# Optimization experiments

Hardware: AMD Instinct MI355X
Metric: run time of the kernel (lower is better)

## Reference

```python
import jax, jax.numpy as jnp
import numpy as np

B, S, H, A = 64, 200, 256, 16
CAPS_LAYERS = 3
NEG = -1e9
LN_EPS = 1e-12


def _layernorm(x, g, b):
    mu = jnp.mean(x, axis=-1, keepdims=True)
    var = jnp.mean(jnp.square(x - mu), axis=-1, keepdims=True)
    return (x - mu) / jnp.sqrt(var + LN_EPS) * g + b


def setup_inputs() -> dict:
    key = jax.random.key(0)
    ks = jax.random.split(key, 10)
    s = 0.02  # initializer_range
    return {
        "item_emb": jax.random.normal(ks[0], (B, S, H), jnp.float32),
        "item_seq": jax.random.randint(ks[1], (B, S), 0, 50000),
        "time_seq": jax.random.randint(ks[2], (B, S, 2), 0, 14),
        "W_lin": s * jax.random.normal(ks[3], (H, H), jnp.float32),
        "b_lin": jnp.zeros((H,), jnp.float32),
        "aspect_embs": s * jax.random.normal(ks[4], (A, H), jnp.float32),
        "pos_emb": s * jax.random.normal(ks[5], (S, H), jnp.float32),
        "tdt_emb": s * jax.random.normal(ks[6], (14, H), jnp.float32),
        "tdn_emb": s * jax.random.normal(ks[7], (14, H), jnp.float32),
        "Wa1": s * jax.random.normal(ks[8], (H, H), jnp.float32),
        "ba1": jnp.zeros((H,), jnp.float32),
        "Wa2": s * jax.random.normal(ks[9], (H,), jnp.float32),
        "ba2": jnp.zeros((1,), jnp.float32),
        "ln_g": jnp.ones((H,), jnp.float32),
        "ln_b": jnp.zeros((H,), jnp.float32),
    }


def reference(item_emb, item_seq, time_seq, W_lin, b_lin, aspect_embs,
              pos_emb, tdt_emb, tdn_emb, Wa1, ba1, Wa2, ba2, ln_g, ln_b):
    b, s = item_emb.shape[0], item_emb.shape[1]
    pad = item_seq == 0  # [B,S]

    # ---- TimeAwareAttention (seq_output has a singleton neighbor dim in torch) ----
    td = tdt_emb[time_seq[:, :, 0]] + tdn_emb[time_seq[:, :, 1]]       # [B,S,H]
    tma_in = pos_emb[None, :s] + item_emb + td                          # [B,S,H]
    h = tma_in @ Wa1 + ba1
    h = jnp.where(h >= 0, h, 0.01 * h)                                  # LeakyReLU
    w = h @ Wa2 + ba2[0]                                                # [B,S]
    w = jnp.where(pad, NEG, w)
    tma = jax.nn.softmax(w, axis=-1)                                    # [B,S]

    # ---- gating (eval: clean gates) ----
    gates = jnp.einsum('bsh,ah->bsa', item_emb, aspect_embs)            # [B,S,A]
    idx = jnp.argmax(gates, axis=-1)                                    # topk k=1, [B,S]

    src = jnp.where(pad, 0.0, 1.0)
    counts = jnp.zeros((b, A), jnp.float32).at[jnp.arange(b)[:, None], idx].add(src)
    aspect_mask = counts == 0                                           # [B,A]

    # ---- item transform (dropout = identity in eval) ----
    moe = _layernorm(jnp.tanh(item_emb @ W_lin + b_lin) + item_emb, ln_g, ln_b)  # [B,S,H]

    # ---- capsule routing ----
    bij = gates
    cap = jnp.broadcast_to(aspect_embs[None], (b, A, H))
    for _ in range(CAPS_LAYERS):
        cij = jnp.where(aspect_mask[:, None, :], NEG, bij)
        cij = jax.nn.softmax(cij, axis=-1)
        cij = jnp.where(pad[:, :, None], 0.0, cij)                      # [B,S,A]
        cap = jnp.einsum('bsa,bsh,bs->bah', cij, moe, tma)              # [B,A,H]
        n2 = jnp.sum(jnp.square(cap), axis=-1, keepdims=True)
        cap = n2 / (1.0 + n2) / jnp.sqrt(n2 + 1e-9) * cap               # squash
        bij = bij + jnp.einsum('bsh,bah->bsa', moe, cap)

    # ---- gather activated interests / activation positions ----
    activated = cap[jnp.arange(b)[:, None], idx]                        # [B,S,H]
    seq_pos = jnp.where(pad, 0, jnp.arange(1, s + 1)[None, :]).astype(jnp.float32)
    act_mat = jnp.full((b, s, A), -1.0, jnp.float32)
    act_mat = act_mat.at[jnp.arange(b)[:, None], jnp.arange(s)[None, :], idx].set(seq_pos)
    act_mat = jnp.where(pad[:, :, None], -1.0, act_mat)
    max_pos = jnp.max(act_mat, axis=1)                                  # [B,A]
    aspects_item_idx = jnp.where(max_pos > -1.0, max_pos - 1.0, max_pos)

    gates_sm = jax.nn.softmax(gates, axis=-1)
    return (cap, gates_sm, aspect_mask, activated, aspects_item_idx, idx[:, :, None])
```

## Files before the change

kernel.cpp:

```cpp
#include <hip/hip_runtime.h>

#define B_ 64
#define S_ 200
#define H_ 256
#define A_ 16
#define M_ (B_*S_)
#define NEGV (-1000000000.0f)

typedef unsigned short ushortT;
typedef __attribute__((ext_vector_type(8))) short short8;
typedef __attribute__((ext_vector_type(4))) float f32x4;

__device__ __forceinline__ ushortT bf16u(float f) {
  unsigned int u = __builtin_bit_cast(unsigned int, f);
  unsigned int r = (u + 0x7fffu + ((u >> 16) & 1u)) >> 16;
  return (ushortT)r;
}
__device__ __forceinline__ float bf2f(ushortT u) {
  unsigned int v = ((unsigned int)u) << 16;
  return __builtin_bit_cast(float, v);
}

__global__ __launch_bounds__(256) void prepT_kernel(
    const float* __restrict__ Wa1, const float* __restrict__ W_lin,
    ushortT* __restrict__ Wa1T, ushortT* __restrict__ WlinT)
{
  __shared__ float T[64*65];
  const int blk = blockIdx.x, t = threadIdx.x;
  int wsel = blk >> 4;
  int tile = blk & 15;
  const float* W = wsel ? W_lin : Wa1;
  ushortT* WT = wsel ? WlinT : Wa1T;
  int tr = (tile >> 2) * 64, tc = (tile & 3) * 64;
  #pragma unroll
  for (int p = 0; p < 16; ++p) {
    int r = p*4 + (t >> 6);
    int c = t & 63;
    T[c*65 + r] = W[(tr + r)*H_ + tc + c];
  }
  __syncthreads();
  #pragma unroll
  for (int p = 0; p < 16; ++p) {
    int n = p*4 + (t >> 6);
    int k = t & 63;
    WT[(tc + n)*H_ + tr + k] = bf16u(T[n*65 + k]);
  }
}

#define ASTR 264
__global__ __launch_bounds__(512) void gemmx_kernel(
    const float* __restrict__ item, const int* __restrict__ iseq,
    const int* __restrict__ tseq, const float* __restrict__ pos,
    const float* __restrict__ tdt, const float* __restrict__ tdn,
    const float* __restrict__ asp,
    const ushortT* __restrict__ Wa1T, const ushortT* __restrict__ WlinT,
    const float* __restrict__ ba1, const float* __restrict__ Wa2,
    const float* __restrict__ ba2, const float* __restrict__ b_lin,
    const float* __restrict__ g_ln, const float* __restrict__ b_ln,
    float* __restrict__ w_out, ushortT* __restrict__ moe_outB,
    float* __restrict__ graw, float* __restrict__ gates_sm,
    float* __restrict__ idxf)
{
  __shared__ __align__(16) ushortT smem[74752];
  __shared__ int sL[64], ttL[64], tnL[64];
  __shared__ float wp[2][64], ln1[2][64], ln2[2][64], mus[64], rss[64];

  const int t = threadIdx.x;

  if (blockIdx.x >= 200) {
    float* aspl = (float*)smem;
    float* gLs  = aspl + 16*260;
    const int m0 = (blockIdx.x - 200) * 32;
    #pragma unroll
    for (int i = 0; i < 2; ++i) {
      int e = t + 512*i;
      int r = e >> 6, c = e & 63;
      *(float4*)&aspl[r*260 + 4*c] = *(const float4*)&asp[r*H_ + 4*c];
    }
    __syncthreads();
    const int r = t >> 4, a = t & 15;
    const int m = m0 + r;
    float g = 0.f;
    #pragma unroll 8
    for (int k4 = 0; k4 < 64; ++k4) {
      float4 xv = *(const float4*)&item[(size_t)m*H_ + 4*k4];
      float4 av = *(const float4*)&aspl[a*260 + 4*k4];
      g += xv.x*av.x + xv.y*av.y + xv.z*av.z + xv.w*av.w;
    }
    gLs[r*20 + a] = g;
    __syncthreads();
    if (t < 128) {
      int rr = t >> 2, q = t & 3;
      float4 gv;
      gv.x = gLs[rr*20 + 4*q + 0]; gv.y = gLs[rr*20 + 4*q + 1];
      gv.z = gLs[rr*20 + 4*q + 2]; gv.w = gLs[rr*20 + 4*q + 3];
      *(float4*)&graw[(m0+rr)*A_ + 4*q] = gv;
    }
    {
      float v = g;
      float mx = v;
      #pragma unroll
      for (int mk = 1; mk < 16; mk <<= 1) mx = fmaxf(mx, __shfl_xor(mx, mk));
      float e = expf(v - mx);
      float sm = e;
      #pragma unroll
      for (int mk = 1; mk < 16; mk <<= 1) sm += __shfl_xor(sm, mk);
      gates_sm[(size_t)m*A_ + a] = e / sm;
    }
    if (t < 32) {
      float best = gLs[t*20]; int bi = 0;
      #pragma unroll
      for (int aa = 1; aa < 16; ++aa) {
        float v = gLs[t*20 + aa];
        if (v > best) { best = v; bi = aa; }
      }
      idxf[m0 + t] = (float)bi;
    }
    return;
  }

  ushortT* Atma = smem;
  ushortT* Aitm = smem + 16896;
  ushortT* Bbuf = smem + 33792;

  const int m0 = blockIdx.x * 64;
  const int lane = t & 63, w = t >> 6;
  const int g = w >> 2, wl = w & 3;
  const int wm = wl >> 1, wn = wl & 1;
  const int col = lane & 15;
  const int rg  = lane >> 4;

  if (t < 64) {
    int m = m0 + t;
    sL[t]  = m % S_;
    ttL[t] = tseq[2*m];
    tnL[t] = tseq[2*m+1];
  }
  __syncthreads();

  const int arow = t >> 3;
  const int ac4  = (t & 7) * 4;
  const int nr   = t >> 1;
  const int kh   = (t & 1) * 16;
  const int srow = sL[arow], trow = ttL[arow], nrow = tnL[arow];

  float4 pi = *(const float4*)&item[(size_t)(m0+arow)*H_ + ac4];
  float4 pp = *(const float4*)&pos[srow*H_ + ac4];
  float4 pt = *(const float4*)&tdt[trow*H_ + ac4];
  float4 pn = *(const float4*)&tdn[nrow*H_ + ac4];
  uint4 b0a = *(const uint4*)&Wa1T[(size_t)nr*H_ + kh];
  uint4 b0b = *(const uint4*)&Wa1T[(size_t)nr*H_ + kh + 8];
  uint4 b1a = *(const uint4*)&WlinT[(size_t)nr*H_ + kh];
  uint4 b1b = *(const uint4*)&WlinT[(size_t)nr*H_ + kh + 8];

  f32x4 acc[2][8];
  #pragma unroll
  for (int r = 0; r < 2; ++r)
    #pragma unroll
    for (int q = 0; q < 8; ++q) acc[r][q] = (f32x4){0.f,0.f,0.f,0.f};

  {
    union { ushortT u[4]; uint2 v; } ci, ct;
    ci.u[0] = bf16u(pi.x); ci.u[1] = bf16u(pi.y);
    ci.u[2] = bf16u(pi.z); ci.u[3] = bf16u(pi.w);
    ct.u[0] = bf16u(pi.x + pp.x + pt.x + pn.x);
    ct.u[1] = bf16u(pi.y + pp.y + pt.y + pn.y);
    ct.u[2] = bf16u(pi.z + pp.z + pt.z + pn.z);
    ct.u[3] = bf16u(pi.w + pp.w + pt.w + pn.w);
    *(uint2*)&Aitm[arow*ASTR + ac4] = ci.v;
    *(uint2*)&Atma[arow*ASTR + ac4] = ct.v;
    *(uint4*)&Bbuf[0*10240 + nr*40 + kh]     = b0a;
    *(uint4*)&Bbuf[0*10240 + nr*40 + kh + 8] = b0b;
    *(uint4*)&Bbuf[2*10240 + nr*40 + kh]     = b1a;
    *(uint4*)&Bbuf[2*10240 + nr*40 + kh + 8] = b1b;
  }
  __syncthreads();

  #pragma unroll
  for (int ks = 0; ks < 8; ++ks) {
    const int k0 = ks*32;
    if (ks < 7) {
      const int k1 = k0 + 32;
      pi = *(const float4*)&item[(size_t)(m0+arow)*H_ + k1 + ac4];
      pp = *(const float4*)&pos[srow*H_ + k1 + ac4];
      pt = *(const float4*)&tdt[trow*H_ + k1 + ac4];
      pn = *(const float4*)&tdn[nrow*H_ + k1 + ac4];
      b0a = *(const uint4*)&Wa1T[(size_t)nr*H_ + k1 + kh];
      b0b = *(const uint4*)&Wa1T[(size_t)nr*H_ + k1 + kh + 8];
      b1a = *(const uint4*)&WlinT[(size_t)nr*H_ + k1 + kh];
      b1b = *(const uint4*)&WlinT[(size_t)nr*H_ + k1 + kh + 8];
    }
    {
      const ushortT* Ab = g ? Aitm : Atma;
      const ushortT* Bb = Bbuf + (g*2 + (ks & 1))*10240;
      short8 af0 = *(const short8*)&Ab[(wm*32 + col)*ASTR + k0 + rg*8];
      short8 af1 = *(const short8*)&Ab[(wm*32 + 16 + col)*ASTR + k0 + rg*8];
      #pragma unroll
      for (int q = 0; q < 8; ++q) {
        short8 bf = *(const short8*)&Bb[(wn*128 + q*16 + col)*40 + rg*8];
        acc[0][q] = __builtin_amdgcn_mfma_f32_16x16x32_bf16(af0, bf, acc[0][q], 0, 0, 0);
        acc[1][q] = __builtin_amdgcn_mfma_f32_16x16x32_bf16(af1, bf, acc[1][q], 0, 0, 0);
      }
    }
    if (ks < 7) {
      const int k1 = k0 + 32;
      const int p = (ks + 1) & 1;
      union { ushortT u[4]; uint2 v; } ci, ct;
      ci.u[0] = bf16u(pi.x); ci.u[1] = bf16u(pi.y);
      ci.u[2] = bf16u(pi.z); ci.u[3] = bf16u(pi.w);
      ct.u[0] = bf16u(pi.x + pp.x + pt.x + pn.x);
      ct.u[1] = bf16u(pi.y + pp.y + pt.y + pn.y);
      ct.u[2] = bf16u(pi.z + pp.z + pt.z + pn.z);
      ct.u[3] = bf16u(pi.w + pp.w + pt.w + pn.w);
      *(uint2*)&Aitm[arow*ASTR + k1 + ac4] = ci.v;
      *(uint2*)&Atma[arow*ASTR + k1 + ac4] = ct.v;
      *(uint4*)&Bbuf[(0*2+p)*10240 + nr*40 + kh]     = b0a;
      *(uint4*)&Bbuf[(0*2+p)*10240 + nr*40 + kh + 8] = b0b;
      *(uint4*)&Bbuf[(1*2+p)*10240 + nr*40 + kh]     = b1a;
      *(uint4*)&Bbuf[(1*2+p)*10240 + nr*40 + kh + 8] = b1b;
    }
    __syncthreads();
  }

  float glv[8], bbv[8];
  if (g == 0) {
    float bav[8], wav[8];
    #pragma unroll
    for (int q = 0; q < 8; ++q) {
      int n = wn*128 + q*16 + col;
      bav[q] = ba1[n]; wav[q] = Wa2[n];
    }
    #pragma unroll
    for (int r = 0; r < 2; ++r)
      #pragma unroll
      for (int j = 0; j < 4; ++j) {
        float p = 0.f;
        #pragma unroll
        for (int q = 0; q < 8; ++q) {
          float h = acc[r][q][j] + bav[q];
          h = (h >= 0.f) ? h : 0.01f*h;
          p += h * wav[q];
        }
        #pragma unroll
        for (int mk = 1; mk < 16; mk <<= 1) p += __shfl_xor(p, mk);
        if (col == 0) wp[wn][wm*32 + r*16 + rg*4 + j] = p;
      }
  } else {
    float blv[8];
    #pragma unroll
    for (int q = 0; q < 8; ++q) {
      int n = wn*128 + q*16 + col;
      blv[q] = b_lin[n]; glv[q] = g_ln[n]; bbv[q] = b_ln[n];
    }
    #pragma unroll
    for (int r = 0; r < 2; ++r)
      #pragma unroll
      for (int j = 0; j < 4; ++j) {
        int row = wm*32 + r*16 + rg*4 + j;
        float s1 = 0.f, s2 = 0.f;
        #pragma unroll
        for (int q = 0; q < 8; ++q) {
          int n = wn*128 + q*16 + col;
          float vv = tanhf(acc[r][q][j] + blv[q]) + bf2f(Aitm[row*ASTR + n]);
          acc[r][q][j] = vv; s1 += vv; s2 += vv*vv;
        }
        #pragma unroll
        for (int mk = 1; mk < 16; mk <<= 1) {
          s1 += __shfl_xor(s1, mk);
          s2 += __shfl_xor(s2, mk);
        }
        if (col == 0) { ln1[wn][row] = s1; ln2[wn][row] = s2; }
      }
  }
  __syncthreads();
  if (t < 64) {
    int row = t, m = m0 + row;
    w_out[m] = (iseq[m] == 0) ? NEGV : (wp[0][row] + wp[1][row] + ba2[0]);
  } else if (t < 128) {
    int row = t - 64;
    float s1 = ln1[0][row] + ln1[1][row];
    float s2 = ln2[0][row] + ln2[1][row];
    float mu  = s1 * (1.0f/H_);
    float var = s2 * (1.0f/H_) - mu*mu;
    mus[row] = mu;
    rss[row] = 1.0f / sqrtf(fmaxf(var, 0.f) + 1e-12f);
  }
  __syncthreads();
  if (g == 1) {
    #pragma unroll
    for (int r = 0; r < 2; ++r)
      #pragma unroll
      for (int j = 0; j < 4; ++j) {
        int row = wm*32 + r*16 + rg*4 + j;
        int m = m0 + row;
        float mu = mus[row], rs = rss[row];
        #pragma unroll
        for (int q = 0; q < 8; ++q) {
          int n = wn*128 + q*16 + col;
          moe_outB[(size_t)m*H_ + n] = bf16u((acc[r][q][j] - mu)*rs*glv[q] + bbv[q]);
        }
      }
  }
}

__device__ __forceinline__ float blk_max(float v, float* red) {
  #pragma unroll
  for (int mk = 32; mk; mk >>= 1) v = fmaxf(v, __shfl_xor(v, mk));
  int t = threadIdx.x;
  if ((t & 63) == 0) red[t >> 6] = v;
  __syncthreads();
  if (t < 64) {
    float x = (t < 16) ? red[t] : -3.0e38f;
    #pragma unroll
    for (int mk = 8; mk; mk >>= 1) x = fmaxf(x, __shfl_xor(x, mk));
    if (t == 0) red[0] = x;
  }
  __syncthreads();
  float r = red[0];
  __syncthreads();
  return r;
}

__device__ __forceinline__ float blk_sum(float v, float* red) {
  #pragma unroll
  for (int mk = 32; mk; mk >>= 1) v += __shfl_xor(v, mk);
  int t = threadIdx.x;
  if ((t & 63) == 0) red[t >> 6] = v;
  __syncthreads();
  if (t < 64) {
    float x = (t < 16) ? red[t] : 0.f;
    #pragma unroll
    for (int mk = 8; mk; mk >>= 1) x += __shfl_xor(x, mk);
    if (t == 0) red[0] = x;
  }
  __syncthreads();
  float r = red[0];
  __syncthreads();
  return r;
}

#define WGSTR 232
#define CBSTR 260
#define CLSTR 252

__global__ __launch_bounds__(1024) void phaseC_kernel(
    const int* __restrict__ iseq, const float* __restrict__ w_in,
    const ushortT* __restrict__ moeB, const float* __restrict__ idxf,
    const float* __restrict__ graw,
    float* __restrict__ cap_out,
    float* __restrict__ mask_out,
    float* __restrict__ aidx_out)
{
  __shared__ ushortT moeTr[57344];
  __shared__ ushortT wgtT[16*WGSTR];
  __shared__ ushortT capB[16*CBSTR];
  __shared__ float bij[4032];
  __shared__ float n2p[16*17];
  __shared__ float n2s[16];
  __shared__ float tmaL[S_];
  __shared__ float red[16];
  __shared__ float maskf[A_];
  __shared__ int counts[A_], maxpos[A_];
  __shared__ int idxl[S_];
  __shared__ int padl[S_];

  const int t = threadIdx.x;
  const int b = blockIdx.x;
  const int base = b * S_;
  const int lane = t & 63, w = t >> 6;
  const int la = lane & 15, lg = lane >> 4;

  #pragma unroll
  for (int u = 0; u < 4; ++u) {
    int e = t + 1024*u;
    if (e < 3584) {
      int ht = e & 15, s = e >> 4;
      int ks = s >> 5, s4l = (s >> 2) & 7, sr = s & 3;
      int bp = (s4l & 1) ? 4 + (s4l >> 1) : (s4l >> 1);
      int li = ((ht*7 + ks)*8 + bp)*64 + sr*16;
      if (s < S_) {
        const ushortT* gp = &moeB[((size_t)(base + s))*H_ + ht*16];
        *(uint4*)&moeTr[li]     = *(const uint4*)gp;
        *(uint4*)&moeTr[li + 8] = *(const uint4*)(gp + 8);
      } else {
        uint4 z = {0,0,0,0};
        *(uint4*)&moeTr[li] = z; *(uint4*)&moeTr[li + 8] = z;
      }
    }
  }
  if (t < 512) {
    int a = t >> 5, s = 200 + (t & 31);
    wgtT[a*WGSTR + s] = 0;
  }

  if (t < A_) { counts[t] = 0; maxpos[t] = -1; }
  float wv = -3.0e38f;
  if (t < S_) {
    int s = t;
    padl[s] = (iseq[base+s] == 0) ? 1 : 0;
    idxl[s] = (int)idxf[base+s];
    wv = w_in[base+s];
    #pragma unroll
    for (int q = 0; q < 4; ++q)
      *(float4*)&bij[s*20 + 4*q] = *(const float4*)&graw[(base+s)*A_ + 4*q];
  }
  __syncthreads();

  short8 a2[7];
  {
    unsigned vA = (unsigned)(w*7168 + lane*8);
    #pragma unroll
    for (int ks = 0; ks < 7; ++ks) {
      long long r0, r1;
      asm volatile(
        "ds_read_b64_tr_b16 %0, %2\n\t"
        "ds_read_b64_tr_b16 %1, %2 offset:512\n\t"
        "s_waitcnt lgkmcnt(0)"
        : "=&v"(r0), "=&v"(r1) : "v"(vA + (unsigned)(ks*1024)) : "memory");
      __builtin_amdgcn_sched_barrier(0);
      union { short8 v; long long q[2]; } uu;
      uu.q[0] = r0; uu.q[1] = r1;
      a2[ks] = uu.v;
    }
  }

  if (t < S_ && !padl[t]) {
    atomicAdd(&counts[idxl[t]], 1);
    atomicMax(&maxpos[idxl[t]], t + 1);
  }
  float mxw = blk_max(wv, red);
  float ev = (t < S_) ? expf(wv - mxw) : 0.f;
  float sw = blk_sum(ev, red);
  if (t < S_) tmaL[t] = ev / sw;
  __syncthreads();
  if (t < A_) {
    int c = counts[t];
    float mkv = (c == 0) ? 1.f : 0.f;
    maskf[t] = mkv;
    mask_out[b*A_ + t] = mkv;
    int mp = maxpos[t];
    aidx_out[b*A_ + t] = (mp > 0) ? (float)(mp - 1) : -1.f;
  }
  __syncthreads();

  for (int iter = 0; iter < 3; ++iter) {
    #pragma unroll
    for (int pass = 0; pass < 4; ++pass) {
      int s = pass*64 + (t >> 4);
      int a = t & 15;
      if (s < S_) {
        float v = bij[s*20 + a];
        v = (maskf[a] > 0.5f) ? NEGV : v;
        float mx = v;
        #pragma unroll
        for (int mk = 1; mk < 16; mk <<= 1) mx = fmaxf(mx, __shfl_xor(mx, mk));
        float e = expf(v - mx);
        float sm = e;
        #pragma unroll
        for (int mk = 1; mk < 16; mk <<= 1) sm += __shfl_xor(sm, mk);
        float sc = (padl[s] ? 0.f : tmaL[s]) / sm;
        wgtT[a*WGSTR + s] = bf16u(e*sc);
      }
    }
    __syncthreads();

    f32x4 acc = (f32x4){0.f,0.f,0.f,0.f};
    #pragma unroll
    for (int ks = 0; ks < 7; ++ks) {
      short8 bf = *(const short8*)&wgtT[la*WGSTR + ks*32 + lg*8];
      acc = __builtin_amdgcn_mfma_f32_16x16x32_bf16(a2[ks], bf, acc, 0, 0, 0);
    }
    {
      float n2 = acc[0]*acc[0] + acc[1]*acc[1] + acc[2]*acc[2] + acc[3]*acc[3];
      n2 += __shfl_xor(n2, 16);
      n2 += __shfl_xor(n2, 32);
      if (lane < 16) n2p[w*17 + lane] = n2;
    }
    __syncthreads();
    if (t < 16) {
      float sv = 0.f;
      #pragma unroll
      for (int w2 = 0; w2 < 16; ++w2) sv += n2p[w2*17 + t];
      n2s[t] = sv / (1.f + sv) / sqrtf(sv + 1e-9f);
    }
    __syncthreads();
    {
      float sc = n2s[la];
      if (iter < 2) {
        #pragma unroll
        for (int r = 0; r < 4; ++r)
          capB[la*CBSTR + w*16 + lg*4 + r] = bf16u(acc[r]*sc);
      } else {
        float* capl = bij;
        #pragma unroll
        for (int r = 0; r < 4; ++r)
          capl[la*CLSTR + w*16 + lg*4 + r] = acc[r]*sc;
      }
    }
    __syncthreads();

    if (iter < 2) {
      if (w < 13) {
        int sR = w*16 + la;
        int ksS = sR >> 5, s4l = (sR >> 2) & 7, sr = sR & 3;
        int bp = (s4l & 1) ? 4 + (s4l >> 1) : (s4l >> 1);
        int laneA = ksS*512 + bp*64 + sr*16 + (lg & 1)*8 + (lg >> 1)*3584;
        f32x4 accS = (f32x4){0.f,0.f,0.f,0.f};
        #pragma unroll
        for (int k4 = 0; k4 < 8; ++k4) {
          short8 am = *(const short8*)&moeTr[laneA + k4*7168];
          short8 bc = *(const short8*)&capB[la*CBSTR + k4*32 + lg*8];
          accS = __builtin_amdgcn_mfma_f32_16x16x32_bf16(am, bc, accS, 0, 0, 0);
        }
        int sW = w*16 + lg*4;
        #pragma unroll
        for (int r = 0; r < 4; ++r)
          if (sW + r < S_) bij[(sW + r)*20 + la] += accS[r];
      }
      __syncthreads();
    }
  }

  {
    const float* capl = bij;
    int a = t >> 6, h4 = t & 63;
    float4 v = *(const float4*)&capl[a*CLSTR + 4*h4];
    *(float4*)&cap_out[((size_t)b*A_ + a)*H_ + 4*h4] = v;
  }
}

__global__ __launch_bounds__(256) void gather_kernel(
    const float* __restrict__ capv, const float* __restrict__ idxf,
    float* __restrict__ act)
{
  int e4 = blockIdx.x * 256 + threadIdx.x;
  int m = e4 >> 6, h4 = e4 & 63;
  int b = m / S_;
  int id = (int)idxf[m];
  float4 v = *(const float4*)&capv[((b*A_) + id)*H_ + 4*h4];
  *(float4*)&act[(size_t)4*e4] = v;
}

extern "C" void kernel_launch(void* const* d_in, const int* in_sizes, int n_in,
                              void* d_out, int out_size, void* d_ws, size_t ws_size,
                              hipStream_t stream) {
  (void)in_sizes; (void)n_in; (void)out_size; (void)ws_size;
  const float* item  = (const float*)d_in[0];
  const int*   iseq  = (const int*)d_in[1];
  const int*   tseq  = (const int*)d_in[2];
  const float* W_lin = (const float*)d_in[3];
  const float* b_lin = (const float*)d_in[4];
  const float* asp   = (const float*)d_in[5];
  const float* pos   = (const float*)d_in[6];
  const float* tdt   = (const float*)d_in[7];
  const float* tdn   = (const float*)d_in[8];
  const float* Wa1   = (const float*)d_in[9];
  const float* ba1   = (const float*)d_in[10];
  const float* Wa2   = (const float*)d_in[11];
  const float* ba2   = (const float*)d_in[12];
  const float* g_ln  = (const float*)d_in[13];
  const float* b_ln  = (const float*)d_in[14];

  float* out    = (float*)d_out;
  float* cap_o  = out;
  float* gate_o = out + 262144;
  float* mask_o = out + 466944;
  float* act_o  = out + 467968;
  float* aidx_o = out + 3744768;
  float* idx_o  = out + 3745792;

  ushortT* moeB  = (ushortT*)d_ws;
  ushortT* Wa1T  = (ushortT*)((char*)d_ws + 6553600);
  ushortT* WlinT = (ushortT*)((char*)d_ws + 6553600 + 131072);
  float*   w_ws  = (float*)((char*)d_ws + 6553600 + 262144);
  float*   graw  = (float*)((char*)d_ws + 6553600 + 262144 + 51200);

  prepT_kernel<<<32, 256, 0, stream>>>(Wa1, W_lin, Wa1T, WlinT);
  gemmx_kernel<<<600, 512, 0, stream>>>(item, iseq, tseq, pos, tdt, tdn, asp,
      Wa1T, WlinT, ba1, Wa2, ba2, b_lin, g_ln, b_ln, w_ws, moeB,
      graw, gate_o, idx_o);
  phaseC_kernel<<<B_, 1024, 0, stream>>>(iseq, w_ws, moeB, idx_o, graw,
      cap_o, mask_o, aidx_o);
  gather_kernel<<<(M_*H_/4)/256, 256, 0, stream>>>(cap_o, idx_o, act_o);
}
```

Before: 60.33 us.

## Fuse gating into GEMM blocks, shrink LDS, fold gather into phaseC

The gating/argmax/softmax work is moved from 400 separate blocks into the tail of each of the 200 GEMM blocks. The A tiles become double-buffered 32-wide K slices instead of full 256-wide rows, which cuts shared memory use. The residual in the epilogue now reads fp32 item from global memory instead of the bf16 LDS copy, which also changes precision slightly. The separate gather kernel is removed and the activated-interest gather is done from LDS at the end of phaseC, saving a launch and a global re-read of cap. The cost is that the gating work now runs serially after the GEMM inside each block, and fewer blocks are launched overall.

Result: faster. 57.95 us (median of 2 runs) (-3.9%).

```diff
diff --git a/kernel.cpp b/kernel.cpp
--- a/kernel.cpp
+++ b/kernel.cpp
@@ -47,8 +47,7 @@
   }
 }
 
-#define ASTR 264
-__global__ __launch_bounds__(512) void gemmx_kernel(
+__global__ __launch_bounds__(512) void fused_kernel(
     const float* __restrict__ item, const int* __restrict__ iseq,
     const int* __restrict__ tseq, const float* __restrict__ pos,
     const float* __restrict__ tdt, const float* __restrict__ tdn,
@@ -61,68 +60,11 @@
     float* __restrict__ graw, float* __restrict__ gates_sm,
     float* __restrict__ idxf)
 {
-  __shared__ __align__(16) ushortT smem[74752];
+  __shared__ __align__(16) ushortT smem[51200];
   __shared__ int sL[64], ttL[64], tnL[64];
   __shared__ float wp[2][64], ln1[2][64], ln2[2][64], mus[64], rss[64];
 
   const int t = threadIdx.x;
-
-  if (blockIdx.x >= 200) {
-    float* aspl = (float*)smem;
-    float* gLs  = aspl + 16*260;
-    const int m0 = (blockIdx.x - 200) * 32;
-    #pragma unroll
-    for (int i = 0; i < 2; ++i) {
-      int e = t + 512*i;
-      int r = e >> 6, c = e & 63;
-      *(float4*)&aspl[r*260 + 4*c] = *(const float4*)&asp[r*H_ + 4*c];
-    }
-    __syncthreads();
-    const int r = t >> 4, a = t & 15;
-    const int m = m0 + r;
-    float g = 0.f;
-    #pragma unroll 8
-    for (int k4 = 0; k4 < 64; ++k4) {
-      float4 xv = *(const float4*)&item[(size_t)m*H_ + 4*k4];
-      float4 av = *(const float4*)&aspl[a*260 + 4*k4];
-      g += xv.x*av.x + xv.y*av.y + xv.z*av.z + xv.w*av.w;
-    }
-    gLs[r*20 + a] = g;
-    __syncthreads();
-    if (t < 128) {
-      int rr = t >> 2, q = t & 3;
-      float4 gv;
-      gv.x = gLs[rr*20 + 4*q + 0]; gv.y = gLs[rr*20 + 4*q + 1];
-      gv.z = gLs[rr*20 + 4*q + 2]; gv.w = gLs[rr*20 + 4*q + 3];
-      *(float4*)&graw[(m0+rr)*A_ + 4*q] = gv;
-    }
-    {
-      float v = g;
-      float mx = v;
-      #pragma unroll
-      for (int mk = 1; mk < 16; mk <<= 1) mx = fmaxf(mx, __shfl_xor(mx, mk));
-      float e = expf(v - mx);
-      float sm = e;
-      #pragma unroll
-      for (int mk = 1; mk < 16; mk <<= 1) sm += __shfl_xor(sm, mk);
-      gates_sm[(size_t)m*A_ + a] = e / sm;
-    }
-    if (t < 32) {
-      float best = gLs[t*20]; int bi = 0;
-      #pragma unroll
-      for (int aa = 1; aa < 16; ++aa) {
-        float v = gLs[t*20 + aa];
-        if (v > best) { best = v; bi = aa; }
-      }
-      idxf[m0 + t] = (float)bi;
-    }
-    return;
-  }
-
-  ushortT* Atma = smem;
-  ushortT* Aitm = smem + 16896;
-  ushortT* Bbuf = smem + 33792;
-
   const int m0 = blockIdx.x * 64;
   const int lane = t & 63, w = t >> 6;
   const int g = w >> 2, wl = w & 3;
@@ -143,6 +85,11 @@
   const int nr   = t >> 1;
   const int kh   = (t & 1) * 16;
   const int srow = sL[arow], trow = ttL[arow], nrow = tnL[arow];
+
+  ushortT* const Atma0 = smem;
+  ushortT* const Aitm0 = smem + 5120;
+  ushortT* const B0b   = smem + 10240;
+  ushortT* const B1b   = smem + 30720;
 
   float4 pi = *(const float4*)&item[(size_t)(m0+arow)*H_ + ac4];
   float4 pp = *(const float4*)&pos[srow*H_ + ac4];
@@ -152,13 +99,6 @@
   uint4 b0b = *(const uint4*)&Wa1T[(size_t)nr*H_ + kh + 8];
   uint4 b1a = *(const uint4*)&WlinT[(size_t)nr*H_ + kh];
   uint4 b1b = *(const uint4*)&WlinT[(size_t)nr*H_ + kh + 8];
-
-  f32x4 acc[2][8];
-  #pragma unroll
-  for (int r = 0; r < 2; ++r)
-    #pragma unroll
-    for (int q = 0; q < 8; ++q) acc[r][q] = (f32x4){0.f,0.f,0.f,0.f};
-
   {
     union { ushortT u[4]; uint2 v; } ci, ct;
     ci.u[0] = bf16u(pi.x); ci.u[1] = bf16u(pi.y);
@@ -167,20 +107,25 @@
     ct.u[1] = bf16u(pi.y + pp.y + pt.y + pn.y);
     ct.u[2] = bf16u(pi.z + pp.z + pt.z + pn.z);
     ct.u[3] = bf16u(pi.w + pp.w + pt.w + pn.w);
-    *(uint2*)&Aitm[arow*ASTR + ac4] = ci.v;
-    *(uint2*)&Atma[arow*ASTR + ac4] = ct.v;
-    *(uint4*)&Bbuf[0*10240 + nr*40 + kh]     = b0a;
-    *(uint4*)&Bbuf[0*10240 + nr*40 + kh + 8] = b0b;
-    *(uint4*)&Bbuf[2*10240 + nr*40 + kh]     = b1a;
-    *(uint4*)&Bbuf[2*10240 + nr*40 + kh + 8] = b1b;
-  }
-  __syncthreads();
+    *(uint2*)&Aitm0[arow*40 + ac4] = ci.v;
+    *(uint2*)&Atma0[arow*40 + ac4] = ct.v;
+    *(uint4*)&B0b[nr*40 + kh]     = b0a;
+    *(uint4*)&B0b[nr*40 + kh + 8] = b0b;
+    *(uint4*)&B1b[nr*40 + kh]     = b1a;
+    *(uint4*)&B1b[nr*40 + kh + 8] = b1b;
+  }
+  __syncthreads();
+
+  f32x4 acc[2][8];
+  #pragma unroll
+  for (int r = 0; r < 2; ++r)
+    #pragma unroll
+    for (int q = 0; q < 8; ++q) acc[r][q] = (f32x4){0.f,0.f,0.f,0.f};
 
   #pragma unroll
   for (int ks = 0; ks < 8; ++ks) {
-    const int k0 = ks*32;
     if (ks < 7) {
-      const int k1 = k0 + 32;
+      const int k1 = (ks + 1) * 32;
       pi = *(const float4*)&item[(size_t)(m0+arow)*H_ + k1 + ac4];
       pp = *(const float4*)&pos[srow*H_ + k1 + ac4];
       pt = *(const float4*)&tdt[trow*H_ + k1 + ac4];
@@ -191,10 +136,11 @@
       b1b = *(const uint4*)&WlinT[(size_t)nr*H_ + k1 + kh + 8];
     }
     {
-      const ushortT* Ab = g ? Aitm : Atma;
-      const ushortT* Bb = Bbuf + (g*2 + (ks & 1))*10240;
-      short8 af0 = *(const short8*)&Ab[(wm*32 + col)*ASTR + k0 + rg*8];
-      short8 af1 = *(const short8*)&Ab[(wm*32 + 16 + col)*ASTR + k0 + rg*8];
+      const int p = ks & 1;
+      const ushortT* Ab = (g ? Aitm0 : Atma0) + p*2560;
+      const ushortT* Bb = (g ? B1b : B0b) + p*10240;
+      short8 af0 = *(const short8*)&Ab[(wm*32 + col)*40 + rg*8];
+      short8 af1 = *(const short8*)&Ab[(wm*32 + 16 + col)*40 + rg*8];
       #pragma unroll
       for (int q = 0; q < 8; ++q) {
         short8 bf = *(const short8*)&Bb[(wn*128 + q*16 + col)*40 + rg*8];
@@ -203,7 +149,6 @@
       }
     }
     if (ks < 7) {
-      const int k1 = k0 + 32;
       const int p = (ks + 1) & 1;
       union { ushortT u[4]; uint2 v; } ci, ct;
       ci.u[0] = bf16u(pi.x); ci.u[1] = bf16u(pi.y);
@@ -212,14 +157,25 @@
       ct.u[1] = bf16u(pi.y + pp.y + pt.y + pn.y);
       ct.u[2] = bf16u(pi.z + pp.z + pt.z + pn.z);
       ct.u[3] = bf16u(pi.w + pp.w + pt.w + pn.w);
-      *(uint2*)&Aitm[arow*ASTR + k1 + ac4] = ci.v;
-      *(uint2*)&Atma[arow*ASTR + k1 + ac4] = ct.v;
-      *(uint4*)&Bbuf[(0*2+p)*10240 + nr*40 + kh]     = b0a;
-      *(uint4*)&Bbuf[(0*2+p)*10240 + nr*40 + kh + 8] = b0b;
-      *(uint4*)&Bbuf[(1*2+p)*10240 + nr*40 + kh]     = b1a;
-      *(uint4*)&Bbuf[(1*2+p)*10240 + nr*40 + kh + 8] = b1b;
+      *(uint2*)&(Aitm0 + p*2560)[arow*40 + ac4] = ci.v;
+      *(uint2*)&(Atma0 + p*2560)[arow*40 + ac4] = ct.v;
+      ushortT* B0w = B0b + p*10240;
+      ushortT* B1w = B1b + p*10240;
+      *(uint4*)&B0w[nr*40 + kh]     = b0a;
+      *(uint4*)&B0w[nr*40 + kh + 8] = b0b;
+      *(uint4*)&B1w[nr*40 + kh]     = b1a;
+      *(uint4*)&B1w[nr*40 + kh + 8] = b1b;
     }
     __syncthreads();
+  }
+
+  float* aspl = (float*)smem;
+  float* gL   = (float*)smem + 4160;
+  #pragma unroll
+  for (int i = 0; i < 2; ++i) {
+    int e = t + 512*i;
+    int r = e >> 6, c = e & 63;
+    *(float4*)&aspl[r*260 + 4*c] = *(const float4*)&asp[r*H_ + 4*c];
   }
 
   float glv[8], bbv[8];
@@ -261,7 +217,7 @@
         #pragma unroll
         for (int q = 0; q < 8; ++q) {
           int n = wn*128 + q*16 + col;
-          float vv = tanhf(acc[r][q][j] + blv[q]) + bf2f(Aitm[row*ASTR + n]);
+          float vv = tanhf(acc[r][q][j] + blv[q]) + item[(size_t)(m0+row)*H_ + n];
           acc[r][q][j] = vv; s1 += vv; s2 += vv*vv;
         }
         #pragma unroll
@@ -301,6 +257,47 @@
         }
       }
   }
+
+  {
+    const int r8 = t >> 3, a2 = (t & 7) * 2;
+    const int m = m0 + r8;
+    float ga = 0.f, gb = 0.f;
+    #pragma unroll 8
+    for (int k4 = 0; k4 < 64; ++k4) {
+      float4 xv = *(const float4*)&item[(size_t)m*H_ + 4*k4];
+      float4 a0 = *(const float4*)&aspl[a2*260 + 4*k4];
+      float4 a1 = *(const float4*)&aspl[(a2+1)*260 + 4*k4];
+      ga += xv.x*a0.x + xv.y*a0.y + xv.z*a0.z + xv.w*a0.w;
+      gb += xv.x*a1.x + xv.y*a1.y + xv.z*a1.z + xv.w*a1.w;
+    }
+    gL[r8*20 + a2]     = ga;
+    gL[r8*20 + a2 + 1] = gb;
+  }
+  __syncthreads();
+  if (t < 64) {
+    float row[16];
+    #pragma unroll
+    for (int a = 0; a < 16; ++a) row[a] = gL[t*20 + a];
+    float best = row[0]; int bi = 0;
+    #pragma unroll
+    for (int a = 1; a < 16; ++a)
+      if (row[a] > best) { best = row[a]; bi = a; }
+    idxf[m0 + t] = (float)bi;
+    float mx = row[0];
+    #pragma unroll
+    for (int a = 1; a < 16; ++a) mx = fmaxf(mx, row[a]);
+    float ex[16], sm = 0.f;
+    #pragma unroll
+    for (int a = 0; a < 16; ++a) { ex[a] = expf(row[a] - mx); sm += ex[a]; }
+    float inv = 1.f / sm;
+    #pragma unroll
+    for (int q = 0; q < 4; ++q) {
+      float4 rv; rv.x = row[4*q]; rv.y = row[4*q+1]; rv.z = row[4*q+2]; rv.w = row[4*q+3];
+      *(float4*)&graw[(m0+t)*A_ + 4*q] = rv;
+      float4 o; o.x = ex[4*q]*inv; o.y = ex[4*q+1]*inv; o.z = ex[4*q+2]*inv; o.w = ex[4*q+3]*inv;
+      *(float4*)&gates_sm[(m0+t)*A_ + 4*q] = o;
+    }
+  }
 }
 
 __device__ __forceinline__ float blk_max(float v, float* red) {
@@ -349,7 +346,8 @@
     const float* __restrict__ graw,
     float* __restrict__ cap_out,
     float* __restrict__ mask_out,
-    float* __restrict__ aidx_out)
+    float* __restrict__ aidx_out,
+    float* __restrict__ act_out)
 {
   __shared__ ushortT moeTr[57344];
   __shared__ ushortT wgtT[16*WGSTR];
@@ -526,19 +524,11 @@
     int a = t >> 6, h4 = t & 63;
     float4 v = *(const float4*)&capl[a*CLSTR + 4*h4];
     *(float4*)&cap_out[((size_t)b*A_ + a)*H_ + 4*h4] = v;
-  }
-}
-
-__global__ __launch_bounds__(256) void gather_kernel(
-    const float* __restrict__ capv, const float* __restrict__ idxf,
-    float* __restrict__ act)
-{
-  int e4 = blockIdx.x * 256 + threadIdx.x;
-  int m = e4 >> 6, h4 = e4 & 63;
-  int b = m / S_;
-  int id = (int)idxf[m];
-  float4 v = *(const float4*)&capv[((b*A_) + id)*H_ + 4*h4];
-  *(float4*)&act[(size_t)4*e4] = v;
+    for (int s = t >> 6; s < S_; s += 16) {
+      float4 av = *(const float4*)&capl[idxl[s]*CLSTR + 4*h4];
+      *(float4*)&act_out[((size_t)base + s)*H_ + 4*h4] = av;
+    }
+  }
 }
 
 extern "C" void kernel_launch(void* const* d_in, const int* in_sizes, int n_in,
@@ -576,10 +566,9 @@
   float*   graw  = (float*)((char*)d_ws + 6553600 + 262144 + 51200);
 
   prepT_kernel<<<32, 256, 0, stream>>>(Wa1, W_lin, Wa1T, WlinT);
-  gemmx_kernel<<<600, 512, 0, stream>>>(item, iseq, tseq, pos, tdt, tdn, asp,
+  fused_kernel<<<200, 512, 0, stream>>>(item, iseq, tseq, pos, tdt, tdn, asp,
       Wa1T, WlinT, ba1, Wa2, ba2, b_lin, g_ln, b_ln, w_ws, moeB,
       graw, gate_o, idx_o);
   phaseC_kernel<<<B_, 1024, 0, stream>>>(iseq, w_ws, moeB, idx_o, graw,
-      cap_o, mask_o, aidx_o);
-  gather_kernel<<<(M_*H_/4)/256, 256, 0, stream>>>(cap_o, idx_o, act_o);
-}
+      cap_o, mask_o, aidx_o, act_o);
+}
```
